# Optimization experiments

Measured on AMD Instinct MI355X. Metric: run time of the kernel, lower is better.

Reference implementation:

```python
import jax, jax.numpy as jnp
import numpy as np

B, D, H0, H1, O = 4096, 1024, 1024, 1024, 1024  # O = output_dim + 1
ALPHA = 0.3
CLAMP = 0.3


def setup_inputs() -> dict:
    key = jax.random.key(0)
    ks = jax.random.split(key, 15)
    def he(k, fan_in, shape):
        return jax.random.normal(k, shape, dtype=jnp.float32) * np.sqrt(2.0 / fan_in).astype(np.float32)
    def heb(k, shape):
        return jax.random.uniform(k, shape, dtype=jnp.float32, minval=-CLAMP, maxval=CLAMP)
    return {
        "x": jax.random.normal(ks[0], (B, D), dtype=jnp.float32),
        "x2h0": he(ks[1], D, (D, H0)),
        "x2h1": he(ks[2], D, (D, H1)),
        "h02h1": he(ks[3], H0, (H0, H1)),
        "x2y": he(ks[4], D, (D, O)),
        "h02y": he(ks[5], H0, (H0, O)),
        "h12y": he(ks[6], H1, (H1, O)),
        "heb_x2h0": heb(ks[7], (D, H0)),
        "heb_x2h1": heb(ks[8], (D, H1)),
        "heb_h02h1": heb(ks[9], (H0, H1)),
        "heb_x2y": heb(ks[10], (D, O)),
        "heb_h02y": heb(ks[11], (H0, O)),
        "heb_h12y": heb(ks[12], (H1, O)),
        "W": jax.random.uniform(ks[13], (1, 1), dtype=jnp.float32),
    }


def reference(x, x2h0, x2h1, h02h1, x2y, h02y, h12y,
              heb_x2h0, heb_x2h1, heb_h02h1, heb_x2y, heb_h02y, heb_h12y, W):
    clamp = lambda m: jnp.clip(m, -CLAMP, CLAMP)
    # x -> h0
    h0_x = x @ (x2h0 + W * heb_x2h0)                       # [B, H0]
    heb_x2h0_n = clamp(heb_x2h0 + ALPHA * (x.T @ h0_x))
    h0 = jax.nn.relu(h0_x)
    # x -> h1, h0 -> h1
    h1_x = x @ (x2h1 + W * heb_x2h1)                       # [B, H1]
    heb_x2h1_n = clamp(heb_x2h1 + ALPHA * (x.T @ h1_x))
    h1_0 = h0 @ (h02h1 + W * heb_h02h1)
    heb_h02h1_n = clamp(heb_h02h1 + ALPHA * (h0.T @ h1_0))
    h1 = jax.nn.relu(h1_x + h1_0)
    # x, h0, h1 -> y
    y_x = x @ (x2y + W * heb_x2y)                          # [B, O]
    heb_x2y_n = clamp(heb_x2y + ALPHA * (x.T @ y_x))
    y_0 = h0 @ (h02y + W * heb_h02y)
    heb_h02y_n = clamp(heb_h02y + ALPHA * (h0.T @ y_0))
    y_1 = h1 @ (h12y + W * heb_h12y)
    heb_h12y_n = clamp(heb_h12y + ALPHA * (h1.T @ y_1))
    y = y_x + y_0 + y_1
    W_new = jnp.mean(jnp.tanh(y[:, -2:-1]))               # neuromodulator scalar
    dopa = jnp.mean(jnp.tanh(y[:, -3:-2]))
    y_out = y[:, :-2]                                      # [B, O-2]
    return (y_out, heb_x2h0_n, heb_x2h1_n, heb_h02h1_n,
            heb_x2y_n, heb_h02y_n, heb_h12y_n, W_new, dopa)
```

## Files before the change

### kernel.cpp

```cpp
#include <hip/hip_runtime.h>
#include <stdint.h>

#define ALPHA 0.3f
#define CLAMPV 0.3f
#define BDIM 4096
#define NDIM 1024

typedef float f32x4 __attribute__((ext_vector_type(4)));
typedef __bf16 bf16x8 __attribute__((ext_vector_type(8)));

union U16x8 { uint4 v; unsigned short u[8]; };

__device__ __forceinline__ float bf2f(unsigned short u) {
  union { unsigned int i; float f; } c; c.i = ((unsigned int)u) << 16; return c.f;
}
__device__ __forceinline__ unsigned short f2bf(float f) {
  union { float f; unsigned int i; } c; c.f = f;
  unsigned int u = c.i;
  unsigned int r = u + 0x7FFFu + ((u >> 16) & 1u);
  return (unsigned short)(r >> 16);
}

__global__ __launch_bounds__(256) void fill_k(float* __restrict__ out, int n) {
  int i = blockIdx.x * 256 + threadIdx.x;
  if (i < n) out[i] = 12345.0f;
}

__global__ __launch_bounds__(256) void split_x_k(const float* __restrict__ x,
                                                 unsigned short* __restrict__ hi,
                                                 unsigned short* __restrict__ lo) {
  const size_t i0 = ((size_t)blockIdx.x * 256 + threadIdx.x) * 8;
  f32x4 a = *(const f32x4*)(x + i0);
  f32x4 b = *(const f32x4*)(x + i0 + 4);
  U16x8 h8, l8;
#pragma unroll
  for (int i = 0; i < 4; ++i) {
    unsigned short h = f2bf(a[i]); h8.u[i] = h; l8.u[i] = f2bf(a[i] - bf2f(h));
    unsigned short h2 = f2bf(b[i]); h8.u[4+i] = h2; l8.u[4+i] = f2bf(b[i] - bf2f(h2));
  }
  *(uint4*)(hi + i0) = h8.v;
  *(uint4*)(lo + i0) = l8.v;
}

struct TDesc {
  const void* in1; const void* in2; const float* Wp;
  unsigned short* out_hi; unsigned short* out_lo;
  int R, C, tilesC, mode;
};
struct TBatch { TDesc d[8]; int start[9]; int n; };

__global__ __launch_bounds__(256) void transpose_k(TBatch batch) {
  const int bid = blockIdx.x;
  int g = 0;
#pragma unroll
  for (int i = 1; i < 8; ++i)
    if (i < batch.n && bid >= batch.start[i]) g = i;
  TDesc D = batch.d[g];
  const int lt = bid - batch.start[g];
  const int trow = lt / D.tilesC;
  const int tcol = lt - trow * D.tilesC;
  const int r0 = trow * 64, c0 = tcol * 64;

  __shared__ float tile[64][65];
  const int t = threadIdx.x;
  const int sub = t >> 3, oct = t & 7;
  const float Wv = (D.mode == 2) ? *D.Wp : 0.f;

#pragma unroll
  for (int p = 0; p < 2; ++p) {
    const int rl = p * 32 + sub;
    const int cl0 = oct * 8;
    float vv[8];
    if (D.mode == 0) {
      const unsigned short* ip = (const unsigned short*)D.in1 + (size_t)(r0 + rl) * D.C + c0 + cl0;
      U16x8 tmp; tmp.v = *(const uint4*)ip;
#pragma unroll
      for (int i = 0; i < 8; ++i) vv[i] = bf2f(tmp.u[i]);
    } else {
      const float* ip = (const float*)D.in1 + (size_t)(r0 + rl) * D.C + c0 + cl0;
      f32x4 a = *(const f32x4*)ip, b = *(const f32x4*)(ip + 4);
#pragma unroll
      for (int i = 0; i < 4; ++i) { vv[i] = a[i]; vv[4+i] = b[i]; }
      if (D.mode == 2) {
        const float* ip2 = (const float*)D.in2 + (size_t)(r0 + rl) * D.C + c0 + cl0;
        f32x4 c = *(const f32x4*)ip2, d2 = *(const f32x4*)(ip2 + 4);
#pragma unroll
        for (int i = 0; i < 4; ++i) { vv[i] += Wv * c[i]; vv[4+i] += Wv * d2[i]; }
      }
    }
#pragma unroll
    for (int i = 0; i < 8; ++i) tile[cl0 + i][rl] = vv[i];
  }
  __syncthreads();
#pragma unroll
  for (int p = 0; p < 2; ++p) {
    const int cl = p * 32 + sub;
    const int rl0 = oct * 8;
    U16x8 h8, l8;
#pragma unroll
    for (int i = 0; i < 8; ++i) {
      float v = tile[cl][rl0 + i];
      unsigned short h = f2bf(v);
      h8.u[i] = h;
      l8.u[i] = f2bf(v - bf2f(h));
    }
    const size_t o = (size_t)(c0 + cl) * D.R + r0 + rl0;
    *(uint4*)(D.out_hi + o) = h8.v;
    if (D.mode != 0) *(uint4*)(D.out_lo + o) = l8.v;
  }
}

struct GemmDesc {
  const unsigned short *Ahi, *Alo, *Bhi, *Blo;
  int lda, ldb, nk, accadd;
  float* out32a;
  float* out32b;
  const float* addin;
  unsigned short* sp_hi;
  unsigned short* sp_lo;
  const float* heb_in;
  float* heb_out;
};
struct GemmBatch { GemmDesc d[12]; int start[13]; int n; };

__global__ __launch_bounds__(256) void gemm_k(GemmBatch batch) {
  const int bid = blockIdx.x;
  int g = 0;
#pragma unroll
  for (int i = 1; i < 12; ++i)
    if (i < batch.n && bid >= batch.start[i]) g = i;
  GemmDesc D = batch.d[g];
  const int local = bid - batch.start[g];
  const int tm = local >> 3;
  const int tn = local & 7;

  __shared__ __align__(16) unsigned short As[128 * 64];
  __shared__ __align__(16) unsigned short BsH[128 * 64];
  __shared__ __align__(16) unsigned short BsL[128 * 64];

  const int t = threadIdx.x;
  const int lane = t & 63;
  const int wave = t >> 6;
  const int wr = wave >> 1, wc = wave & 1;
  const int fr = lane & 15, fg = lane >> 4;

  const f32x4 vzero = {0.f, 0.f, 0.f, 0.f};
  f32x4 acc[4][4];
#pragma unroll
  for (int i = 0; i < 4; ++i)
#pragma unroll
    for (int j = 0; j < 4; ++j) acc[i][j] = vzero;

  const int srow = t >> 3;
  const int scolB = ((t & 7) << 4) ^ ((srow & 7) << 4);
  const int scolE = scolB >> 1;

  int aoff[4], boff[4];
#pragma unroll
  for (int i = 0; i < 4; ++i) {
    const int ra = wr * 64 + i * 16 + fr;
    aoff[i] = ra * 128 + ((fg << 4) ^ ((ra & 7) << 4));
    const int rb = wc * 64 + i * 16 + fr;
    boff[i] = rb * 128 + ((fg << 4) ^ ((rb & 7) << 4));
  }
  const char* Asb = (const char*)As;
  const char* BsHb = (const char*)BsH;
  const char* BsLb = (const char*)BsL;

  const size_t arow = (size_t)(tm * 128 + srow) * D.lda + scolE;
  const size_t brow = (size_t)(tn * 128 + srow) * D.ldb + scolE;
  const size_t astep = (size_t)32 * D.lda;
  const size_t bstep = (size_t)32 * D.ldb;

#pragma unroll 1
  for (int ph = 0; ph < 2; ++ph) {
    const unsigned short* Ap = ph ? D.Alo : D.Ahi;
#pragma unroll 1
    for (int kt = 0; kt < D.nk; ++kt) {
      const int kb = kt << 6;
#pragma unroll
      for (int q = 0; q < 4; ++q) {
        __builtin_amdgcn_global_load_lds(
            (const __attribute__((address_space(1))) void*)(Ap + arow + q * astep + kb),
            (__attribute__((address_space(3))) void*)(As + q * 2048 + wave * 512), 16, 0, 0);
        __builtin_amdgcn_global_load_lds(
            (const __attribute__((address_space(1))) void*)(D.Bhi + brow + q * bstep + kb),
            (__attribute__((address_space(3))) void*)(BsH + q * 2048 + wave * 512), 16, 0, 0);
      }
      if (ph == 0) {
#pragma unroll
        for (int q = 0; q < 4; ++q)
          __builtin_amdgcn_global_load_lds(
              (const __attribute__((address_space(1))) void*)(D.Blo + brow + q * bstep + kb),
              (__attribute__((address_space(3))) void*)(BsL + q * 2048 + wave * 512), 16, 0, 0);
      }
      __syncthreads();
#pragma unroll
      for (int s = 0; s < 2; ++s) {
        const int sx = s << 6;
        bf16x8 af[4];
#pragma unroll
        for (int i = 0; i < 4; ++i) af[i] = *(const bf16x8*)(Asb + (aoff[i] ^ sx));
#pragma unroll
        for (int j = 0; j < 4; ++j) {
          const bf16x8 bh = *(const bf16x8*)(BsHb + (boff[j] ^ sx));
#pragma unroll
          for (int i = 0; i < 4; ++i)
            acc[i][j] = __builtin_amdgcn_mfma_f32_16x16x32_bf16(af[i], bh, acc[i][j], 0, 0, 0);
          if (ph == 0) {
            const bf16x8 bl = *(const bf16x8*)(BsLb + (boff[j] ^ sx));
#pragma unroll
            for (int i = 0; i < 4; ++i)
              acc[i][j] = __builtin_amdgcn_mfma_f32_16x16x32_bf16(af[i], bl, acc[i][j], 0, 0, 0);
          }
        }
      }
      __syncthreads();
    }
  }

  const int grb = tm * 128 + wr * 64 + fg * 4;
  const int gcb = tn * 128 + wc * 64 + fr;
#pragma unroll
  for (int i = 0; i < 4; ++i) {
#pragma unroll
    for (int j = 0; j < 4; ++j) {
      const int gc = gcb + j * 16;
#pragma unroll
      for (int r = 0; r < 4; ++r) {
        const int gr = grb + i * 16 + r;
        const size_t idx = (size_t)gr * NDIM + gc;
        const float v = acc[i][j][r];
        if (D.heb_out) {
          D.heb_out[idx] = fminf(fmaxf(D.heb_in[idx] + ALPHA * v, -CLAMPV), CLAMPV);
        } else {
          if (D.out32a) D.out32a[idx] = v;
          if (D.out32b) D.out32b[idx] = D.accadd ? (D.out32b[idx] + v) : v;
          if (D.sp_hi) {
            float rv = v + (D.addin ? D.addin[idx] : 0.f);
            rv = fmaxf(rv, 0.f);
            const unsigned short h = f2bf(rv);
            D.sp_hi[idx] = h;
            D.sp_lo[idx] = f2bf(rv - bf2f(h));
          }
        }
      }
    }
  }
}

struct HebRed { const float* heb_in; float* out; const float* p[8]; int np; };

__global__ __launch_bounds__(256) void hebred_k(HebRed R) {
  const size_t i0 = ((size_t)blockIdx.x * 256 + threadIdx.x) * 4;
  f32x4 s = *(const f32x4*)(R.p[0] + i0);
#pragma unroll
  for (int k = 1; k < 8; ++k)
    if (k < R.np) s += *(const f32x4*)(R.p[k] + i0);
  f32x4 h = *(const f32x4*)(R.heb_in + i0);
  f32x4 o;
#pragma unroll
  for (int i = 0; i < 4; ++i) o[i] = fminf(fmaxf(h[i] + ALPHA * s[i], -CLAMPV), CLAMPV);
  *(f32x4*)(R.out + i0) = o;
}

__global__ __launch_bounds__(256) void yassm_k(const float* __restrict__ ysum,
                                               float* __restrict__ yout) {
  const int stride = gridDim.x * 256;
  for (int idx = blockIdx.x * 256 + threadIdx.x; idx < BDIM * 1022; idx += stride) {
    const int row = idx / 1022;
    const int col = idx - row * 1022;
    yout[idx] = ysum[(size_t)row * NDIM + col];
  }
}

__global__ __launch_bounds__(256) void tanhcol_k(const float* __restrict__ ysum,
                                                 float* __restrict__ wpart,
                                                 float* __restrict__ dpart) {
  const int r = blockIdx.x * 256 + threadIdx.x;
  const size_t b = (size_t)r * NDIM;
  float tw = tanhf(ysum[b + 1022]);
  float td = tanhf(ysum[b + 1021]);
#pragma unroll
  for (int o = 32; o > 0; o >>= 1) { tw += __shfl_down(tw, o); td += __shfl_down(td, o); }
  __shared__ float s1[4], s2[4];
  const int lane = threadIdx.x & 63, wv = threadIdx.x >> 6;
  if (lane == 0) { s1[wv] = tw; s2[wv] = td; }
  __syncthreads();
  if (threadIdx.x == 0) {
    wpart[blockIdx.x] = s1[0] + s1[1] + s1[2] + s1[3];
    dpart[blockIdx.x] = s2[0] + s2[1] + s2[2] + s2[3];
  }
}

__global__ void finalize_k(const float* __restrict__ wpart, const float* __restrict__ dpart,
                           float* __restrict__ out, int nout) {
  if (threadIdx.x == 0 && blockIdx.x == 0) {
    float s = 0.f, d = 0.f;
    for (int i = 0; i < 16; ++i) { s += wpart[i]; d += dpart[i]; }
    out[nout - 2] = s * (1.f / BDIM);
    out[nout - 1] = d * (1.f / BDIM);
  }
}

extern "C" void kernel_launch(void* const* d_in, const int* in_sizes, int n_in,
                              void* d_out, int out_size, void* d_ws, size_t ws_size,
                              hipStream_t stream) {
  const float* x = (const float*)d_in[0];
  const float* wbase[6]; const float* hebin[6];
  for (int i = 0; i < 6; ++i) { wbase[i] = (const float*)d_in[1 + i]; hebin[i] = (const float*)d_in[7 + i]; }
  const float* Wp = (const float*)d_in[13];
  float* out = (float*)d_out;
  const size_t YOUT = (size_t)BDIM * 1022;
  float* hebout[6];
  for (int i = 0; i < 6; ++i) hebout[i] = out + YOUT + (size_t)i * 1048576;

  const size_t E = (size_t)BDIM * NDIM;
  const size_t PAIRB = E * 4;
  const size_t WPAIRB = (size_t)NDIM * NDIM * 4;
  const size_t FB = E * 4;
  const size_t REQUIRED = 7 * PAIRB + 6 * WPAIRB + 4 * FB;

  if (ws_size < REQUIRED) {
    fill_k<<<(out_size + 255) / 256, 256, 0, stream>>>(out, out_size);
    return;
  }

  char* p = (char*)d_ws;
  auto takeB = [&](size_t n) -> char* { char* q = p; p += n; return q; };

  unsigned short* R0 = (unsigned short*)takeB(PAIRB);
  unsigned short* R1 = (unsigned short*)takeB(PAIRB);
  unsigned short* R2 = (unsigned short*)takeB(PAIRB);
  unsigned short* R3 = (unsigned short*)takeB(PAIRB);
  unsigned short* R4 = (unsigned short*)takeB(PAIRB);
  unsigned short* R5 = (unsigned short*)takeB(PAIRB);
  unsigned short* R6 = (unsigned short*)takeB(PAIRB);
  unsigned short* WThi[6]; unsigned short* WTlo[6];
  for (int i = 0; i < 6; ++i) {
    WThi[i] = (unsigned short*)takeB(WPAIRB);
    WTlo[i] = WThi[i] + (size_t)NDIM * NDIM;
  }
  float* F0 = (float*)takeB(FB);
  float* F1 = (float*)takeB(FB);
  float* F2 = (float*)takeB(FB);
  float* F3 = (float*)takeB(FB);

  unsigned short *xhi = R0, *xlo = R0 + E;
  unsigned short *xThi = R1, *xTlo = R1 + E;
  unsigned short *h0hi = R2, *h0lo = R2 + E;
  unsigned short *h0Thi = R3, *h0Tlo = R3 + E;
  float* part = (float*)R4;
  float* wpart = (float*)R6; float* dpart = wpart + 64;

  split_x_k<<<2048, 256, 0, stream>>>(x, xhi, xlo);

  {
    TBatch tb{};
    int s = 0;
    for (int i = 0; i < 6; ++i) {
      tb.d[i] = { wbase[i], hebin[i], Wp, WThi[i], WTlo[i], NDIM, NDIM, NDIM / 64, 2 };
      tb.start[i] = s; s += (NDIM / 64) * (NDIM / 64);
    }
    tb.d[6] = { x, nullptr, nullptr, xThi, xTlo, BDIM, NDIM, NDIM / 64, 1 };
    tb.start[6] = s; s += (BDIM / 64) * (NDIM / 64);
    tb.start[7] = s; tb.n = 7;
    transpose_k<<<s, 256, 0, stream>>>(tb);
  }

  auto fwdDesc = [&](const unsigned short* ahi, const unsigned short* alo, int wi) -> GemmDesc {
    GemmDesc d{};
    d.Ahi = ahi; d.Alo = alo; d.Bhi = WThi[wi]; d.Blo = WTlo[wi];
    d.lda = NDIM; d.ldb = NDIM; d.nk = NDIM / 64;
    return d;
  };
  auto hebPart = [&](const unsigned short* ahi, const unsigned short* alo,
                     const unsigned short* bhi, const unsigned short* blo,
                     int koff, int klen, float* partOut) -> GemmDesc {
    GemmDesc d{};
    d.Ahi = ahi + koff; d.Alo = alo + koff;
    d.Bhi = bhi + koff; d.Blo = blo + koff;
    d.lda = BDIM; d.ldb = BDIM; d.nk = klen / 64;
    d.out32a = partOut;
    return d;
  };
  auto hebRed = [&](int hi, const float* q0, const float* q1, const float* q2,
                    const float* q3, const float* q4, const float* q5,
                    const float* q6, const float* q7, int np) {
    HebRed r{};
    r.heb_in = hebin[hi]; r.out = hebout[hi];
    r.p[0]=q0; r.p[1]=q1; r.p[2]=q2; r.p[3]=q3; r.p[4]=q4; r.p[5]=q5; r.p[6]=q6; r.p[7]=q7;
    r.np = np;
    hebred_k<<<1024, 256, 0, stream>>>(r);
  };

  {
    GemmBatch gb{};
    gb.d[0] = fwdDesc(xhi, xlo, 0);
    gb.d[0].out32a = F0; gb.d[0].sp_hi = h0hi; gb.d[0].sp_lo = h0lo;
    gb.d[1] = fwdDesc(xhi, xlo, 1);
    gb.d[1].out32a = F1;
    gb.d[2] = fwdDesc(xhi, xlo, 3);
    gb.d[2].out32a = F2; gb.d[2].out32b = F3; gb.d[2].accadd = 0;
    gb.start[0] = 0; gb.start[1] = 256; gb.start[2] = 512; gb.start[3] = 768;
    gb.n = 3;
    gemm_k<<<768, 256, 0, stream>>>(gb);
  }

  {
    TBatch tb{};
    tb.d[0] = { F0, nullptr, nullptr, R4, R4 + E, BDIM, NDIM, NDIM / 64, 1 };
    tb.d[1] = { F1, nullptr, nullptr, R5, R5 + E, BDIM, NDIM, NDIM / 64, 1 };
    tb.d[2] = { F2, nullptr, nullptr, R6, R6 + E, BDIM, NDIM, NDIM / 64, 1 };
    tb.d[3] = { h0hi, nullptr, nullptr, h0Thi, nullptr, BDIM, NDIM, NDIM / 64, 0 };
    tb.d[4] = { h0lo, nullptr, nullptr, h0Tlo, nullptr, BDIM, NDIM, NDIM / 64, 0 };
    for (int i = 0; i < 6; ++i) tb.start[i] = i * 1024;
    tb.n = 5;
    transpose_k<<<5120, 256, 0, stream>>>(tb);
  }

  {
    float* px0a = (float*)WThi[0]; float* px0b = hebout[0];
    float* px1a = (float*)WThi[1]; float* px1b = hebout[1];
    float* pxya = (float*)WThi[3]; float* pxyb = hebout[3];
    GemmBatch gb{};
    gb.d[0] = hebPart(xThi, xTlo, R4, R4 + E, 0,    2048, px0a);
    gb.d[1] = hebPart(xThi, xTlo, R4, R4 + E, 2048, 2048, px0b);
    gb.d[2] = hebPart(xThi, xTlo, R5, R5 + E, 0,    2048, px1a);
    gb.d[3] = hebPart(xThi, xTlo, R5, R5 + E, 2048, 2048, px1b);
    gb.d[4] = hebPart(xThi, xTlo, R6, R6 + E, 0,    2048, pxya);
    gb.d[5] = hebPart(xThi, xTlo, R6, R6 + E, 2048, 2048, pxyb);
    gb.d[6] = fwdDesc(h0hi, h0lo, 2);
    gb.d[6].out32a = F0; gb.d[6].addin = F1; gb.d[6].sp_hi = R0; gb.d[6].sp_lo = R0 + E;
    gb.d[7] = fwdDesc(h0hi, h0lo, 4);
    gb.d[7].out32a = F2; gb.d[7].out32b = F3; gb.d[7].accadd = 1;
    for (int i = 0; i < 6; ++i) gb.start[i] = i * 64;
    gb.start[6] = 384; gb.start[7] = 640; gb.start[8] = 896;
    gb.n = 8;
    gemm_k<<<896, 256, 0, stream>>>(gb);
    hebRed(0, px0a, px0b, 0,0,0,0,0,0, 2);
    hebRed(1, px1a, px1b, 0,0,0,0,0,0, 2);
    hebRed(3, pxya, pxyb, 0,0,0,0,0,0, 2);
  }

  {
    TBatch tb{};
    tb.d[0] = { F0, nullptr, nullptr, R4, R4 + E, BDIM, NDIM, NDIM / 64, 1 };
    tb.d[1] = { F2, nullptr, nullptr, R5, R5 + E, BDIM, NDIM, NDIM / 64, 1 };
    tb.d[2] = { R0, nullptr, nullptr, R1, nullptr, BDIM, NDIM, NDIM / 64, 0 };
    tb.d[3] = { R0 + E, nullptr, nullptr, R1 + E, nullptr, BDIM, NDIM, NDIM / 64, 0 };
    for (int i = 0; i < 5; ++i) tb.start[i] = i * 1024;
    tb.n = 4;
    transpose_k<<<4096, 256, 0, stream>>>(tb);
  }

  {
    float* pa[4] = { (float*)WThi[0], (float*)WThi[1], (float*)WThi[2], (float*)WThi[3] };
    float* pb[4] = { (float*)R6, (float*)R6 + 1048576, (float*)R6 + 2097152, (float*)R6 + 3145728 };
    GemmBatch gb{};
    for (int h = 0; h < 4; ++h) {
      gb.d[h]     = hebPart(h0Thi, h0Tlo, R4, R4 + E, h * 1024, 1024, pa[h]);
      gb.d[4 + h] = hebPart(h0Thi, h0Tlo, R5, R5 + E, h * 1024, 1024, pb[h]);
    }
    gb.d[8] = fwdDesc(R0, R0 + E, 5);
    gb.d[8].out32a = F1; gb.d[8].out32b = F3; gb.d[8].accadd = 1;
    for (int i = 0; i < 8; ++i) gb.start[i] = i * 64;
    gb.start[8] = 512; gb.start[9] = 768;
    gb.n = 9;
    gemm_k<<<768, 256, 0, stream>>>(gb);
    hebRed(2, pa[0], pa[1], pa[2], pa[3], 0,0,0,0, 4);
    hebRed(4, pb[0], pb[1], pb[2], pb[3], 0,0,0,0, 4);
  }

  {
    TBatch tb{};
    tb.d[0] = { F1, nullptr, nullptr, R2, R2 + E, BDIM, NDIM, NDIM / 64, 1 };
    tb.start[0] = 0; tb.start[1] = 1024; tb.n = 1;
    transpose_k<<<1024, 256, 0, stream>>>(tb);
  }

  {
    GemmBatch gb{};
    for (int h = 0; h < 8; ++h)
      gb.d[h] = hebPart(R1, R1 + E, R2, R2 + E, h * 512, 512, part + (size_t)h * 1048576);
    for (int i = 0; i <= 8; ++i) gb.start[i] = i * 64;
    gb.n = 8;
    gemm_k<<<512, 256, 0, stream>>>(gb);
    hebRed(5, part, part + 1048576, part + 2097152, part + 3145728,
           part + 4194304, part + 5242880, part + 6291456, part + 7340032, 8);
  }

  yassm_k<<<2048, 256, 0, stream>>>(F3, out);
  tanhcol_k<<<16, 256, 0, stream>>>(F3, wpart, dpart);
  finalize_k<<<1, 64, 0, stream>>>(wpart, dpart, out, out_size);
}
```

Baseline: 502.2 us.

## Double-buffer GEMM LDS staging with 256x128 tiles and BK=32

Rewrites the split-bf16 GEMM main loop to double-buffer the LDS tiles, issuing the next k-step's global-to-LDS loads before computing the current one with explicit vmcnt waits. The block tile grows from 128x128 to 256x128 (8x4 MFMA fragments per wave) and the K step shrinks from 64 to 32 with a new swizzle, and grid sizes are halved to match. The aim is to hide global load latency behind MFMA work and improve data reuse per block. In exchange each block uses more accumulator registers and there are fewer blocks per launch, which may leave some CUs underused on the smaller batches.

```diff
diff --git a/kernel.cpp b/kernel.cpp
--- a/kernel.cpp
+++ b/kernel.cpp
@@ -123,7 +123,10 @@
 };
 struct GemmBatch { GemmDesc d[12]; int start[13]; int n; };
 
-__global__ __launch_bounds__(256) void gemm_k(GemmBatch batch) {
+#define AS1 __attribute__((address_space(1)))
+#define AS3 __attribute__((address_space(3)))
+
+__global__ __launch_bounds__(256, 2) void gemm_k(GemmBatch batch) {
   const int bid = blockIdx.x;
   int g = 0;
 #pragma unroll
@@ -134,9 +137,7 @@
   const int tm = local >> 3;
   const int tn = local & 7;
 
-  __shared__ __align__(16) unsigned short As[128 * 64];
-  __shared__ __align__(16) unsigned short BsH[128 * 64];
-  __shared__ __align__(16) unsigned short BsL[128 * 64];
+  __shared__ __align__(16) unsigned short LDS[32768];
 
   const int t = threadIdx.x;
   const int lane = t & 63;
@@ -144,85 +145,135 @@
   const int wr = wave >> 1, wc = wave & 1;
   const int fr = lane & 15, fg = lane >> 4;
 
-  const f32x4 vzero = {0.f, 0.f, 0.f, 0.f};
-  f32x4 acc[4][4];
-#pragma unroll
-  for (int i = 0; i < 4; ++i)
-#pragma unroll
-    for (int j = 0; j < 4; ++j) acc[i][j] = vzero;
-
-  const int srow = t >> 3;
-  const int scolB = ((t & 7) << 4) ^ ((srow & 7) << 4);
-  const int scolE = scolB >> 1;
-
-  int aoff[4], boff[4];
-#pragma unroll
-  for (int i = 0; i < 4; ++i) {
-    const int ra = wr * 64 + i * 16 + fr;
-    aoff[i] = ra * 128 + ((fg << 4) ^ ((ra & 7) << 4));
-    const int rb = wc * 64 + i * 16 + fr;
-    boff[i] = rb * 128 + ((fg << 4) ^ ((rb & 7) << 4));
-  }
-  const char* Asb = (const char*)As;
-  const char* BsHb = (const char*)BsH;
-  const char* BsLb = (const char*)BsL;
-
-  const size_t arow = (size_t)(tm * 128 + srow) * D.lda + scolE;
-  const size_t brow = (size_t)(tn * 128 + srow) * D.ldb + scolE;
-  const size_t astep = (size_t)32 * D.lda;
-  const size_t bstep = (size_t)32 * D.ldb;
+  f32x4 acc[8][4];
+#pragma unroll
+  for (int i = 0; i < 8; ++i)
+#pragma unroll
+    for (int j = 0; j < 4; ++j)
+#pragma unroll
+      for (int r = 0; r < 4; ++r) acc[i][j][r] = 0.f;
+
+  const int r0 = t >> 2;
+  const int colSwE = (((t & 3) ^ ((t >> 3) & 3)) << 3);
+
+  size_t aRow[4], bRow[2];
+#pragma unroll
+  for (int q = 0; q < 4; ++q)
+    aRow[q] = (size_t)(tm * 256 + q * 64 + r0) * D.lda + colSwE;
+#pragma unroll
+  for (int q = 0; q < 2; ++q)
+    bRow[q] = (size_t)(tn * 128 + q * 64 + r0) * D.ldb + colSwE;
+
+  const int ldsW = wave * 512;
+
+  auto stageA = [&](const unsigned short* P, int kb, int b) {
+    unsigned short* base = LDS + b * 16384 + ldsW;
+#pragma unroll
+    for (int q = 0; q < 4; ++q)
+      __builtin_amdgcn_global_load_lds(
+          (const AS1 void*)(P + aRow[q] + kb),
+          (AS3 void*)(base + q * 2048), 16, 0, 0);
+  };
+  auto stageB = [&](const unsigned short* P, int region, int kb, int b) {
+    unsigned short* base = LDS + b * 16384 + region + ldsW;
+#pragma unroll
+    for (int q = 0; q < 2; ++q)
+      __builtin_amdgcn_global_load_lds(
+          (const AS1 void*)(P + bRow[q] + kb),
+          (AS3 void*)(base + q * 2048), 16, 0, 0);
+  };
+
+  const int swz = ((fg ^ ((fr >> 1) & 3)) << 4);
+  int aoff[8], boff[4];
+#pragma unroll
+  for (int i = 0; i < 8; ++i)
+    aoff[i] = (wr * 128 + i * 16 + fr) * 64 + swz;
+#pragma unroll
+  for (int j = 0; j < 4; ++j)
+    boff[j] = 16384 + (wc * 64 + j * 16 + fr) * 64 + swz;
+  const char* ldsc = (const char*)LDS;
+
+  auto computePh0 = [&](int b) {
+    const char* bb = ldsc + b * 32768;
+    bf16x8 af[8];
+#pragma unroll
+    for (int i = 0; i < 8; ++i) af[i] = *(const bf16x8*)(bb + aoff[i]);
+#pragma unroll
+    for (int j = 0; j < 4; ++j) {
+      const bf16x8 bh = *(const bf16x8*)(bb + boff[j]);
+#pragma unroll
+      for (int i = 0; i < 8; ++i)
+        acc[i][j] = __builtin_amdgcn_mfma_f32_16x16x32_bf16(af[i], bh, acc[i][j], 0, 0, 0);
+      const bf16x8 bl = *(const bf16x8*)(bb + boff[j] + 8192);
+#pragma unroll
+      for (int i = 0; i < 8; ++i)
+        acc[i][j] = __builtin_amdgcn_mfma_f32_16x16x32_bf16(af[i], bl, acc[i][j], 0, 0, 0);
+    }
+  };
+  auto computePh1 = [&](int b) {
+    const char* bb = ldsc + b * 32768;
+    bf16x8 af[8];
+#pragma unroll
+    for (int i = 0; i < 8; ++i) af[i] = *(const bf16x8*)(bb + aoff[i]);
+#pragma unroll
+    for (int j = 0; j < 4; ++j) {
+      const bf16x8 bh = *(const bf16x8*)(bb + boff[j]);
+#pragma unroll
+      for (int i = 0; i < 8; ++i)
+        acc[i][j] = __builtin_amdgcn_mfma_f32_16x16x32_bf16(af[i], bh, acc[i][j], 0, 0, 0);
+    }
+  };
+
+  const int n = D.nk;
+
+  stageA(D.Ahi, 0, 0);
+  stageB(D.Bhi, 8192, 0, 0);
+  stageB(D.Blo, 12288, 0, 0);
+  int buf = 0;
 
 #pragma unroll 1
-  for (int ph = 0; ph < 2; ++ph) {
-    const unsigned short* Ap = ph ? D.Alo : D.Ahi;
+  for (int kt = 0; kt < n; ++kt) {
+    if (kt + 1 < n) {
+      const int kb = (kt + 1) << 5;
+      stageA(D.Ahi, kb, buf ^ 1);
+      stageB(D.Bhi, 8192, kb, buf ^ 1);
+      stageB(D.Blo, 12288, kb, buf ^ 1);
+      asm volatile("s_waitcnt vmcnt(8)" ::: "memory");
+    } else {
+      stageA(D.Alo, 0, buf ^ 1);
+      stageB(D.Bhi, 8192, 0, buf ^ 1);
+      asm volatile("s_waitcnt vmcnt(6)" ::: "memory");
+    }
+    __builtin_amdgcn_s_barrier();
+    __builtin_amdgcn_sched_barrier(0);
+    computePh0(buf);
+    __builtin_amdgcn_sched_barrier(0);
+    __builtin_amdgcn_s_barrier();
+    buf ^= 1;
+  }
+
 #pragma unroll 1
-    for (int kt = 0; kt < D.nk; ++kt) {
-      const int kb = kt << 6;
-#pragma unroll
-      for (int q = 0; q < 4; ++q) {
-        __builtin_amdgcn_global_load_lds(
-            (const __attribute__((address_space(1))) void*)(Ap + arow + q * astep + kb),
-            (__attribute__((address_space(3))) void*)(As + q * 2048 + wave * 512), 16, 0, 0);
-        __builtin_amdgcn_global_load_lds(
-            (const __attribute__((address_space(1))) void*)(D.Bhi + brow + q * bstep + kb),
-            (__attribute__((address_space(3))) void*)(BsH + q * 2048 + wave * 512), 16, 0, 0);
-      }
-      if (ph == 0) {
-#pragma unroll
-        for (int q = 0; q < 4; ++q)
-          __builtin_amdgcn_global_load_lds(
-              (const __attribute__((address_space(1))) void*)(D.Blo + brow + q * bstep + kb),
-              (__attribute__((address_space(3))) void*)(BsL + q * 2048 + wave * 512), 16, 0, 0);
-      }
-      __syncthreads();
-#pragma unroll
-      for (int s = 0; s < 2; ++s) {
-        const int sx = s << 6;
-        bf16x8 af[4];
-#pragma unroll
-        for (int i = 0; i < 4; ++i) af[i] = *(const bf16x8*)(Asb + (aoff[i] ^ sx));
-#pragma unroll
-        for (int j = 0; j < 4; ++j) {
-          const bf16x8 bh = *(const bf16x8*)(BsHb + (boff[j] ^ sx));
-#pragma unroll
-          for (int i = 0; i < 4; ++i)
-            acc[i][j] = __builtin_amdgcn_mfma_f32_16x16x32_bf16(af[i], bh, acc[i][j], 0, 0, 0);
-          if (ph == 0) {
-            const bf16x8 bl = *(const bf16x8*)(BsLb + (boff[j] ^ sx));
-#pragma unroll
-            for (int i = 0; i < 4; ++i)
-              acc[i][j] = __builtin_amdgcn_mfma_f32_16x16x32_bf16(af[i], bl, acc[i][j], 0, 0, 0);
-          }
-        }
-      }
-      __syncthreads();
-    }
-  }
-
-  const int grb = tm * 128 + wr * 64 + fg * 4;
+  for (int kt = 0; kt < n; ++kt) {
+    if (kt + 1 < n) {
+      const int kb = (kt + 1) << 5;
+      stageA(D.Alo, kb, buf ^ 1);
+      stageB(D.Bhi, 8192, kb, buf ^ 1);
+      asm volatile("s_waitcnt vmcnt(6)" ::: "memory");
+    } else {
+      asm volatile("s_waitcnt vmcnt(0)" ::: "memory");
+    }
+    __builtin_amdgcn_s_barrier();
+    __builtin_amdgcn_sched_barrier(0);
+    computePh1(buf);
+    __builtin_amdgcn_sched_barrier(0);
+    __builtin_amdgcn_s_barrier();
+    buf ^= 1;
+  }
+
+  const int grb = tm * 256 + wr * 128 + fg * 4;
   const int gcb = tn * 128 + wc * 64 + fr;
 #pragma unroll
-  for (int i = 0; i < 4; ++i) {
+  for (int i = 0; i < 8; ++i) {
 #pragma unroll
     for (int j = 0; j < 4; ++j) {
       const int gc = gcb + j * 16;
@@ -371,7 +422,7 @@
   auto fwdDesc = [&](const unsigned short* ahi, const unsigned short* alo, int wi) -> GemmDesc {
     GemmDesc d{};
     d.Ahi = ahi; d.Alo = alo; d.Bhi = WThi[wi]; d.Blo = WTlo[wi];
-    d.lda = NDIM; d.ldb = NDIM; d.nk = NDIM / 64;
+    d.lda = NDIM; d.ldb = NDIM; d.nk = NDIM / 32;
     return d;
   };
   auto hebPart = [&](const unsigned short* ahi, const unsigned short* alo,
@@ -380,7 +431,7 @@
     GemmDesc d{};
     d.Ahi = ahi + koff; d.Alo = alo + koff;
     d.Bhi = bhi + koff; d.Blo = blo + koff;
-    d.lda = BDIM; d.ldb = BDIM; d.nk = klen / 64;
+    d.lda = BDIM; d.ldb = BDIM; d.nk = klen / 32;
     d.out32a = partOut;
     return d;
   };
@@ -402,9 +453,9 @@
     gb.d[1].out32a = F1;
     gb.d[2] = fwdDesc(xhi, xlo, 3);
     gb.d[2].out32a = F2; gb.d[2].out32b = F3; gb.d[2].accadd = 0;
-    gb.start[0] = 0; gb.start[1] = 256; gb.start[2] = 512; gb.start[3] = 768;
+    gb.start[0] = 0; gb.start[1] = 128; gb.start[2] = 256; gb.start[3] = 384;
     gb.n = 3;
-    gemm_k<<<768, 256, 0, stream>>>(gb);
+    gemm_k<<<384, 256, 0, stream>>>(gb);
   }
 
   {
@@ -434,10 +485,10 @@
     gb.d[6].out32a = F0; gb.d[6].addin = F1; gb.d[6].sp_hi = R0; gb.d[6].sp_lo = R0 + E;
     gb.d[7] = fwdDesc(h0hi, h0lo, 4);
     gb.d[7].out32a = F2; gb.d[7].out32b = F3; gb.d[7].accadd = 1;
-    for (int i = 0; i < 6; ++i) gb.start[i] = i * 64;
-    gb.start[6] = 384; gb.start[7] = 640; gb.start[8] = 896;
+    for (int i = 0; i < 6; ++i) gb.start[i] = i * 32;
+    gb.start[6] = 192; gb.start[7] = 320; gb.start[8] = 448;
     gb.n = 8;
-    gemm_k<<<896, 256, 0, stream>>>(gb);
+    gemm_k<<<448, 256, 0, stream>>>(gb);
     hebRed(0, px0a, px0b, 0,0,0,0,0,0, 2);
     hebRed(1, px1a, px1b, 0,0,0,0,0,0, 2);
     hebRed(3, pxya, pxyb, 0,0,0,0,0,0, 2);
@@ -464,10 +515,10 @@
     }
     gb.d[8] = fwdDesc(R0, R0 + E, 5);
     gb.d[8].out32a = F1; gb.d[8].out32b = F3; gb.d[8].accadd = 1;
-    for (int i = 0; i < 8; ++i) gb.start[i] = i * 64;
-    gb.start[8] = 512; gb.start[9] = 768;
+    for (int i = 0; i < 8; ++i) gb.start[i] = i * 32;
+    gb.start[8] = 256; gb.start[9] = 384;
     gb.n = 9;
-    gemm_k<<<768, 256, 0, stream>>>(gb);
+    gemm_k<<<384, 256, 0, stream>>>(gb);
     hebRed(2, pa[0], pa[1], pa[2], pa[3], 0,0,0,0, 4);
     hebRed(4, pb[0], pb[1], pb[2], pb[3], 0,0,0,0, 4);
   }
@@ -483,9 +534,9 @@
     GemmBatch gb{};
     for (int h = 0; h < 8; ++h)
       gb.d[h] = hebPart(R1, R1 + E, R2, R2 + E, h * 512, 512, part + (size_t)h * 1048576);
-    for (int i = 0; i <= 8; ++i) gb.start[i] = i * 64;
+    for (int i = 0; i <= 8; ++i) gb.start[i] = i * 32;
     gb.n = 8;
-    gemm_k<<<512, 256, 0, stream>>>(gb);
+    gemm_k<<<256, 256, 0, stream>>>(gb);
     hebRed(5, part, part + 1048576, part + 2097152, part + 3145728,
            part + 4194304, part + 5242880, part + 6291456, part + 7340032, 8);
   }
```

Measured after the change: 513.2 us. 2.2% more time.
